# Performance work log

Hardware: AMD Instinct MI355X
Metric: run time of the kernel (lower is better)

The kernel has to match this reference:

```python
import jax, jax.numpy as jnp
import numpy as np

DIM = 256
NEG_SLOPE = 0.01  # torch F.leaky_relu default


def setup_inputs() -> dict:
    key = jax.random.key(0)
    ks = jax.random.split(key, 10)
    B, O, I, D = 16, 64, 512, DIM
    q = jax.random.normal(ks[0], (B, O, D), dtype=jnp.float32)
    k = jax.random.normal(ks[1], (B, I, D), dtype=jnp.float32)
    v = jax.random.normal(ks[2], (B, I, D), dtype=jnp.float32)
    mask = jax.random.randint(ks[3], (B, I), 0, 2).astype(bool)  # 1/True = pad
    s = 1.0 / np.sqrt(2 * D)
    # score MLP: Linear(2D -> D), tanh, Linear(D -> 1)
    W1 = jax.random.normal(ks[4], (D, 2 * D), dtype=jnp.float32) * s
    b1 = jnp.zeros((D,), dtype=jnp.float32)
    W2 = jax.random.normal(ks[5], (1, D), dtype=jnp.float32) * (1.0 / np.sqrt(D))
    b2 = jnp.zeros((1,), dtype=jnp.float32)
    # output projection fw: Linear(D -> D)
    Wf = jax.random.normal(ks[6], (D, D), dtype=jnp.float32) * (1.0 / np.sqrt(D))
    bf = jnp.zeros((D,), dtype=jnp.float32)
    return {"q": q, "k": k, "v": v, "mask": mask,
            "W1": W1, "b1": b1, "W2": W2, "b2": b2, "Wf": Wf, "bf": bf}


def reference(q, k, v, mask, W1, b1, W2, b2, Wf, bf):
    # Linear over concat([q, k]) decomposes exactly: W1 @ [q;k] = W1q@q + W1k@k
    D = q.shape[-1]
    W1q, W1k = W1[:, :D], W1[:, D:]
    qp = jnp.einsum('bod,hd->boh', q, W1q)          # (B, O, D)
    kp = jnp.einsum('bid,hd->bih', k, W1k)          # (B, I, D)
    h = jnp.tanh(qp[:, :, None, :] + kp[:, None, :, :] + b1)  # (B, O, I, D)
    score = jnp.einsum('boih,h->boi', h, W2[0]) + b2[0]       # (B, O, I)
    score = jnp.where(mask[:, None, :], -jnp.inf, score)
    attn = jax.nn.softmax(score, axis=-1)           # (B, O, I)
    out = jnp.einsum('boi,bid->bod', attn, v)       # (B, O, D)
    out = out @ Wf.T + bf                           # dropout in eval mode = identity
    out = jnp.where(out >= 0, out, NEG_SLOPE * out) # leaky_relu
    return out, attn
```

## Files before the change

kernel.cpp:

```cpp
#include <hip/hip_runtime.h>
#include <math.h>

#define DIM 256
#define BATCH 16
#define NO 64
#define NI 512
#define NIP 528
#define WFT_LD 272
#define NEG_SLOPE 0.01f
#define CSCALE 2.885390081777927f
#define OT 2

typedef float f32x4 __attribute__((ext_vector_type(4)));
typedef __bf16 bf16x8 __attribute__((ext_vector_type(8)));
typedef unsigned int u32x4 __attribute__((ext_vector_type(4)));

__device__ __forceinline__ void split2(float f, unsigned int& hi16, float& lo) {
  unsigned int u = __builtin_bit_cast(unsigned int, f);
  unsigned int h = (u + 0x7FFFu + ((u >> 16) & 1u)) & 0xFFFF0000u;
  hi16 = h >> 16;
  lo = f - __builtin_bit_cast(float, h);
}
__device__ __forceinline__ unsigned int rne16(float f) {
  unsigned int u = __builtin_bit_cast(unsigned int, f);
  return (u + 0x7FFFu + ((u >> 16) & 1u)) >> 16;
}

struct __align__(8) U2 { unsigned int x, y; };

#define OFF_AH 0
#define OFF_AL 9216
#define OFF_WH 18432
#define OFF_WL 27648

__global__ __launch_bounds__(256, 4) void proj_kernel(
    const float* __restrict__ q, const float* __restrict__ k,
    const float* __restrict__ W1, const float* __restrict__ b1,
    const float* __restrict__ Wf, const int* __restrict__ mask,
    float* __restrict__ Eq, float* __restrict__ Ek4, float* __restrict__ WfT)
{
  __shared__ __align__(16) char smemRaw[36864];
  __shared__ int idx_s[64];
  __shared__ int swtot[4];

  const int t  = threadIdx.x;
  const int bx = blockIdx.x;

  if (bx >= 576) {
    float* smem = (float*)smemRaw;
    const int tt = bx - 576;
    const int tr = tt >> 2, tc = tt & 3;
#pragma unroll
    for (int p = 0; p < 4; ++p) {
      int idx2 = p * 256 + t;
      int row = idx2 >> 4, j = idx2 & 15;
      float4 vv = *(const float4*)(Wf + (size_t)(tr * 64 + row) * 256 + tc * 64 + j * 4);
      *(float4*)&smem[row * 68 + j * 4] = vv;
    }
    __syncthreads();
#pragma unroll
    for (int p = 0; p < 4; ++p) {
      int idx2 = p * 256 + t;
      int row = idx2 >> 4, j = idx2 & 15;
      float4 ov;
      ov.x = smem[(j * 4 + 0) * 68 + row];
      ov.y = smem[(j * 4 + 1) * 68 + row];
      ov.z = smem[(j * 4 + 2) * 68 + row];
      ov.w = smem[(j * 4 + 3) * 68 + row];
      *(float4*)(WfT + (size_t)(tc * 64 + row) * WFT_LD + tr * 64 + j * 4) = ov;
    }
    return;
  }

  const int mt = bx >> 2;
  const int nt = bx & 3;
  const int h0 = nt * 64;
  const bool isq = (mt < 16);

  const int srow = t >> 4;
  const int sc4  = t & 15;
  const int lane = t & 63, w = t >> 6;
  const int m0w = (w >> 1) * 32, n0w = (w & 1) * 32;
  const int lr = lane & 15, lg = lane >> 4;

  const float* src;
  int coff, bb = 0, jb0 = 0, cntb = 0;
  int rowg[4];

  if (isq) {
    src  = q + (size_t)(mt * 64) * DIM;
    coff = 0;
#pragma unroll
    for (int p = 0; p < 4; ++p) rowg[p] = srow + p * 16;
  } else {
    const int ki = mt - 16;
    bb  = ki >> 3;
    jb0 = (ki & 7) * 64;
    const int e0 = (mask[bb * NI + 2 * t] == 0);
    const int e1 = (mask[bb * NI + 2 * t + 1] == 0);
    const int ps = e0 + e1;
    int x = ps;
#pragma unroll
    for (int off = 1; off < 64; off <<= 1) {
      int y = __shfl_up(x, off, 64);
      if (lane >= off) x += y;
    }
    if (lane == 63) swtot[w] = x;
    if (t < 64) idx_s[t] = 0;
    __syncthreads();
    int woffv = 0;
#pragma unroll
    for (int w2 = 0; w2 < 4; ++w2) {
      int v_ = swtot[w2];
      if (w2 < w) woffv += v_;
      cntb += v_;
    }
    const int excl = woffv + x - ps;
    const int p0 = excl, p1 = excl + e0;
    if (e0 && p0 >= jb0 && p0 < jb0 + 64) idx_s[p0 - jb0] = 2 * t;
    if (e1 && p1 >= jb0 && p1 < jb0 + 64) idx_s[p1 - jb0] = 2 * t + 1;
    __syncthreads();
    if (jb0 >= cntb) return;
    src  = k + (size_t)bb * NI * DIM;
    coff = DIM;
#pragma unroll
    for (int p = 0; p < 4; ++p) rowg[p] = idx_s[srow + p * 16];
  }

  f32x4 acc[2][2] = {};

  float4 aR[4], wR[4];
#define LOADC(c0_)                                                              \
  _Pragma("unroll")                                                             \
  for (int p = 0; p < 4; ++p) {                                                 \
    aR[p] = *(const float4*)(src + (size_t)rowg[p] * DIM + (c0_) + sc4 * 4);    \
    wR[p] = *(const float4*)(W1 + (size_t)(h0 + srow + p * 16) * (2 * DIM) + coff + (c0_) + sc4 * 4); \
  }

  LOADC(0)

  for (int c = 0; c < 4; ++c) {
#pragma unroll
    for (int p = 0; p < 4; ++p) {
      int row = srow + p * 16;
      int boff = row * 144 + sc4 * 8;
      unsigned int h0_, h1_, h2_, h3_;
      float l0, l1, l2, l3;
      split2(aR[p].x, h0_, l0); split2(aR[p].y, h1_, l1);
      split2(aR[p].z, h2_, l2); split2(aR[p].w, h3_, l3);
      *(U2*)(smemRaw + OFF_AH + boff) = { h0_ | (h1_ << 16), h2_ | (h3_ << 16) };
      *(U2*)(smemRaw + OFF_AL + boff) = { rne16(l0) | (rne16(l1) << 16),
                                          rne16(l2) | (rne16(l3) << 16) };
      split2(wR[p].x, h0_, l0); split2(wR[p].y, h1_, l1);
      split2(wR[p].z, h2_, l2); split2(wR[p].w, h3_, l3);
      *(U2*)(smemRaw + OFF_WH + boff) = { h0_ | (h1_ << 16), h2_ | (h3_ << 16) };
      *(U2*)(smemRaw + OFF_WL + boff) = { rne16(l0) | (rne16(l1) << 16),
                                          rne16(l2) | (rne16(l3) << 16) };
    }
    __syncthreads();

    if (c < 3) { LOADC((c + 1) * 64) }

#pragma unroll
    for (int kk = 0; kk < 2; ++kk) {
      const int kb = kk * 64 + lg * 16;
      bf16x8 ah[2], al[2], bh[2], bl[2];
#pragma unroll
      for (int mi = 0; mi < 2; ++mi) {
        int row = m0w + mi * 16 + lr;
        ah[mi] = __builtin_bit_cast(bf16x8, *(const u32x4*)(smemRaw + OFF_AH + row * 144 + kb));
        al[mi] = __builtin_bit_cast(bf16x8, *(const u32x4*)(smemRaw + OFF_AL + row * 144 + kb));
      }
#pragma unroll
      for (int ni = 0; ni < 2; ++ni) {
        int row = n0w + ni * 16 + lr;
        bh[ni] = __builtin_bit_cast(bf16x8, *(const u32x4*)(smemRaw + OFF_WH + row * 144 + kb));
        bl[ni] = __builtin_bit_cast(bf16x8, *(const u32x4*)(smemRaw + OFF_WL + row * 144 + kb));
      }
#pragma unroll
      for (int mi = 0; mi < 2; ++mi)
#pragma unroll
        for (int ni = 0; ni < 2; ++ni) {
          acc[mi][ni] = __builtin_amdgcn_mfma_f32_16x16x32_bf16(ah[mi], bh[ni], acc[mi][ni], 0, 0, 0);
          acc[mi][ni] = __builtin_amdgcn_mfma_f32_16x16x32_bf16(ah[mi], bl[ni], acc[mi][ni], 0, 0, 0);
          acc[mi][ni] = __builtin_amdgcn_mfma_f32_16x16x32_bf16(al[mi], bh[ni], acc[mi][ni], 0, 0, 0);
        }
    }
    __syncthreads();
  }

  if (isq) {
    const int r0 = mt * 64;
#pragma unroll
    for (int ni = 0; ni < 2; ++ni) {
      int h = h0 + n0w + ni * 16 + lr;
      float b1v = b1[h];
#pragma unroll
      for (int mi = 0; mi < 2; ++mi)
#pragma unroll
        for (int rg = 0; rg < 4; ++rg) {
          int r = r0 + m0w + mi * 16 + lg * 4 + rg;
          Eq[(size_t)r * DIM + h] =
              __builtin_amdgcn_exp2f((acc[mi][ni][rg] + b1v) * CSCALE);
        }
    }
  } else {
    const int lim = cntb - jb0;
#pragma unroll
    for (int mi = 0; mi < 2; ++mi)
#pragma unroll
      for (int rg = 0; rg < 4; ++rg) {
        int local = m0w + mi * 16 + lg * 4 + rg;
        if (local < lim) {
          int pos = jb0 + local;
#pragma unroll
          for (int ni = 0; ni < 2; ++ni) {
            int h = h0 + n0w + ni * 16 + lr;
            Ek4[((size_t)(bb * 64 + (h >> 2)) * NIP + pos) * 4 + (h & 3)] =
                __builtin_amdgcn_exp2f(acc[mi][ni][rg] * CSCALE);
          }
        }
      }
  }
}

__device__ __forceinline__ void f4arr(float4 v, float* a) {
  a[0] = v.x; a[1] = v.y; a[2] = v.z; a[3] = v.w;
}

__global__ __launch_bounds__(512, 4) void attn_kernel(
    const float* __restrict__ Eq, const float* __restrict__ Ek4,
    const float* __restrict__ v, const int* __restrict__ mask,
    const float* __restrict__ W2, const float* __restrict__ b2,
    const float* __restrict__ WfT, const float* __restrict__ bf,
    float* __restrict__ out, float* __restrict__ attn_out)
{
  __shared__ float sc[OT][NI];
  __shared__ int   idxs[NI];
  __shared__ float qs[OT][DIM];
  __shared__ float w2s[DIM];
  __shared__ float pvp[8][OT][DIM];
  __shared__ float o0[OT][DIM];
  __shared__ float red4[8][OT];
  __shared__ float redw[8];
  __shared__ int   swtot8[8];

  const int t    = threadIdx.x;
  const int lane = t & 63;
  const int wid  = t >> 6;

  const int blk  = blockIdx.x;
  const int tile = (blk & 7) * 64 + (blk >> 3);
  const int b    = tile >> 5;
  const int bo0  = b * 64 + (tile & 31) * OT;

  const int unm = (mask[b * NI + t] == 0) ? 1 : 0;
  unsigned long long bal = __ballot(unm);
  int my = __popcll(bal & ((1ull << lane) - 1ull));
  if (lane == 0) swtot8[wid] = __popcll(bal);

  if (t < 128) {
    const int r = t >> 6, part = t & 63;
    *(float4*)&qs[r][part * 4] =
        *(const float4*)(Eq + (size_t)(bo0 + r) * DIM + part * 4);
  } else if (t < 192) {
    const int part = t - 128;
    *(float4*)&w2s[part * 4] = *(const float4*)(W2 + part * 4);
  }

  float partial = (t < DIM) ? W2[t] : 0.f;
#pragma unroll
  for (int off = 32; off >= 1; off >>= 1) partial += __shfl_xor(partial, off, 64);
  if (lane == 0) redw[wid] = partial;
  __syncthreads();

  int cntb = 0, woffv = 0;
#pragma unroll
  for (int w = 0; w < 8; ++w) {
    int v_ = swtot8[w];
    if (w < wid) woffv += v_;
    cntb += v_;
  }
  const int myPos = unm ? (woffv + my) : -1;
  if (unm) idxs[myPos] = t;

  float sumw2 = 0.f;
#pragma unroll
  for (int w = 0; w < 8; ++w) sumw2 += redw[w];
  const float base = sumw2 + b2[0];

  const int j = t;
  const bool active = (j < cntb);
  const int jc = active ? j : (cntb > 0 ? cntb - 1 : 0);
  const float4* kb4 = (const float4*)Ek4 + (size_t)b * 64 * NIP;

  float acc0 = 0.f, acc1 = 0.f;
  if (wid * 64 < cntb) {
    const float4* kp = kb4 + jc;
#pragma unroll
    for (int c0 = 0; c0 < 64; c0 += 16) {
      float4 kqr[16];
#pragma unroll
      for (int u = 0; u < 16; ++u)
        kqr[u] = kp[(size_t)(c0 + u) * NIP];
#pragma unroll
      for (int u = 0; u < 16; ++u) {
        const int hq = c0 + u;
        float wr[4], q0r[4], q1r[4], kv[4];
        f4arr(*(const float4*)&w2s[hq * 4], wr);
        f4arr(*(const float4*)&qs[0][hq * 4], q0r);
        f4arr(*(const float4*)&qs[1][hq * 4], q1r);
        f4arr(kqr[u], kv);
#pragma unroll
        for (int pr = 0; pr < 2; ++pr) {
          const int ea = pr * 2, eb = pr * 2 + 1;
          float A0 = fmaf(q0r[ea], kv[ea], 1.f);
          float B0 = fmaf(q0r[eb], kv[eb], 1.f);
          float N0 = fmaf(wr[eb], A0, wr[ea] * B0);
          acc0 = fmaf(N0, __builtin_amdgcn_rcpf(A0 * B0), acc0);
          float A1 = fmaf(q1r[ea], kv[ea], 1.f);
          float B1 = fmaf(q1r[eb], kv[eb], 1.f);
          float N1 = fmaf(wr[eb], A1, wr[ea] * B1);
          acc1 = fmaf(N1, __builtin_amdgcn_rcpf(A1 * B1), acc1);
        }
      }
    }
  }

  float s0 = active ? (base - 2.f * acc0) : -INFINITY;
  float s1 = active ? (base - 2.f * acc1) : -INFINITY;

  float p0 = __builtin_amdgcn_exp2f(s0 * 1.4426950408889634f);
  float p1 = __builtin_amdgcn_exp2f(s1 * 1.4426950408889634f);
  float ps0 = p0, ps1 = p1;
#pragma unroll
  for (int off = 32; off >= 1; off >>= 1) {
    ps0 += __shfl_xor(ps0, off, 64);
    ps1 += __shfl_xor(ps1, off, 64);
  }
  __syncthreads();
  if (lane == 0) { red4[wid][0] = ps0; red4[wid][1] = ps1; }
  __syncthreads();
  float ss0 = 0.f, ss1 = 0.f;
#pragma unroll
  for (int w = 0; w < 8; ++w) { ss0 += red4[w][0]; ss1 += red4[w][1]; }
  const float a0 = p0 * __builtin_amdgcn_rcpf(ss0);
  const float a1 = p1 * __builtin_amdgcn_rcpf(ss1);
  sc[0][j] = a0;
  sc[1][j] = a1;
  __syncthreads();

  {
    float w0 = (myPos >= 0) ? sc[0][myPos] : 0.f;
    float w1 = (myPos >= 0) ? sc[1][myPos] : 0.f;
    attn_out[(size_t)(bo0 + 0) * NI + t] = w0;
    attn_out[(size_t)(bo0 + 1) * NI + t] = w1;
  }

  {
    const int d4 = lane;
    float4 av0 = {0.f, 0.f, 0.f, 0.f};
    float4 av1 = {0.f, 0.f, 0.f, 0.f};
    const float4* vb4 = (const float4*)(v + (size_t)b * NI * DIM);
    const int jstart = wid * 64;
    const int jend = min(jstart + 64, cntb);
    int jb = jstart;
    for (; jb + 8 <= jend; jb += 8) {
      float4 vr[8];
      float sa0[8], sa1[8];
#pragma unroll
      for (int u = 0; u < 8; ++u) {
        int row = idxs[jb + u];
        vr[u] = vb4[(size_t)row * 64 + d4];
        sa0[u] = sc[0][jb + u];
        sa1[u] = sc[1][jb + u];
      }
#pragma unroll
      for (int u = 0; u < 8; ++u) {
        av0.x = fmaf(sa0[u], vr[u].x, av0.x);
        av0.y = fmaf(sa0[u], vr[u].y, av0.y);
        av0.z = fmaf(sa0[u], vr[u].z, av0.z);
        av0.w = fmaf(sa0[u], vr[u].w, av0.w);
        av1.x = fmaf(sa1[u], vr[u].x, av1.x);
        av1.y = fmaf(sa1[u], vr[u].y, av1.y);
        av1.z = fmaf(sa1[u], vr[u].z, av1.z);
        av1.w = fmaf(sa1[u], vr[u].w, av1.w);
      }
    }
    for (; jb < jend; ++jb) {
      int row = idxs[jb];
      float sa0 = sc[0][jb], sa1 = sc[1][jb];
      float4 vv = vb4[(size_t)row * 64 + d4];
      av0.x = fmaf(sa0, vv.x, av0.x);
      av0.y = fmaf(sa0, vv.y, av0.y);
      av0.z = fmaf(sa0, vv.z, av0.z);
      av0.w = fmaf(sa0, vv.w, av0.w);
      av1.x = fmaf(sa1, vv.x, av1.x);
      av1.y = fmaf(sa1, vv.y, av1.y);
      av1.z = fmaf(sa1, vv.z, av1.z);
      av1.w = fmaf(sa1, vv.w, av1.w);
    }
    *(float4*)&pvp[wid][0][d4 * 4] = av0;
    *(float4*)&pvp[wid][1][d4 * 4] = av1;
  }
  __syncthreads();
  {
    int oo = t >> 8, d = t & 255;
    float sacc = 0.f;
#pragma unroll
    for (int w = 0; w < 8; ++w) sacc += pvp[w][oo][d];
    o0[oo][d] = sacc;
  }
  __syncthreads();

  if (t < DIM) {
    const int d = t;
    float f0 = 0.f, f1 = 0.f;
#pragma unroll
    for (int c0 = 0; c0 < 256; c0 += 16) {
      float wv[16];
#pragma unroll
      for (int u = 0; u < 16; ++u)
        wv[u] = WfT[(size_t)(c0 + u) * WFT_LD + d];
#pragma unroll
      for (int u = 0; u < 16; ++u) {
        f0 = fmaf(o0[0][c0 + u], wv[u], f0);
        f1 = fmaf(o0[1][c0 + u], wv[u], f1);
      }
    }
    float bfv = bf[d];
    f0 += bfv; f1 += bfv;
    f0 = (f0 >= 0.f) ? f0 : NEG_SLOPE * f0;
    f1 = (f1 >= 0.f) ? f1 : NEG_SLOPE * f1;
    out[(size_t)(bo0 + 0) * DIM + d] = f0;
    out[(size_t)(bo0 + 1) * DIM + d] = f1;
  }
}

extern "C" void kernel_launch(void* const* d_in, const int* in_sizes, int n_in,
                              void* d_out, int out_size, void* d_ws, size_t ws_size,
                              hipStream_t stream) {
  const float* q    = (const float*)d_in[0];
  const float* k    = (const float*)d_in[1];
  const float* v    = (const float*)d_in[2];
  const int*   mask = (const int*)d_in[3];
  const float* W1   = (const float*)d_in[4];
  const float* b1   = (const float*)d_in[5];
  const float* W2   = (const float*)d_in[6];
  const float* b2   = (const float*)d_in[7];
  const float* Wf   = (const float*)d_in[8];
  const float* bf   = (const float*)d_in[9];

  float* out      = (float*)d_out;
  float* attn_out = out + (size_t)BATCH * NO * DIM;

  float* Eq   = (float*)d_ws;
  float* Ek4  = Eq + (size_t)BATCH * NO * DIM;
  float* WfT  = Ek4 + (size_t)BATCH * 64 * NIP * 4;

  proj_kernel<<<592, 256, 0, stream>>>(q, k, W1, b1, Wf, mask, Eq, Ek4, WfT);
  attn_kernel<<<(BATCH * NO) / OT, 512, 0, stream>>>(Eq, Ek4, v, mask,
                                                     W2, b2, WfT, bf, out, attn_out);
}
```

Measured before the change: 121.8 us.

## Fuse projection and attention kernels into one persistent kernel with grid barrier

Merges the projection kernel and the attention kernel into a single 512-block launch. Each block first computes one or two projection tiles, reshaped for 512 threads, then waits on an atomic grid-wide barrier before running the attention phase. The goal is to remove the second kernel launch and the gap between the two kernels. The cost is a spin barrier that relies on all 512 blocks being co-resident, plus an extra memset launch and agent-scope stores.

```diff
diff --git a/kernel.cpp b/kernel.cpp
--- a/kernel.cpp
+++ b/kernel.cpp
@@ -10,6 +10,7 @@
 #define NEG_SLOPE 0.01f
 #define CSCALE 2.885390081777927f
 #define OT 2
+#define NBLK 512
 
 typedef float f32x4 __attribute__((ext_vector_type(4)));
 typedef __bf16 bf16x8 __attribute__((ext_vector_type(8)));
@@ -25,6 +26,12 @@
   unsigned int u = __builtin_bit_cast(unsigned int, f);
   return (u + 0x7FFFu + ((u >> 16) & 1u)) >> 16;
 }
+__device__ __forceinline__ void st_agent(float* p, float v) {
+  __hip_atomic_store(p, v, __ATOMIC_RELAXED, __HIP_MEMORY_SCOPE_AGENT);
+}
+__device__ __forceinline__ void f4arr(float4 v, float* a) {
+  a[0] = v.x; a[1] = v.y; a[2] = v.z; a[3] = v.w;
+}
 
 struct __align__(8) U2 { unsigned int x, y; };
 
@@ -32,130 +39,126 @@
 #define OFF_AL 9216
 #define OFF_WH 18432
 #define OFF_WL 27648
-
-__global__ __launch_bounds__(256, 4) void proj_kernel(
+#define OFF_IDX 36864
+#define OFF_SWT 37120
+
+__device__ void proj_tile(
+    int L, char* SMEM, int t, int lane, int wid,
     const float* __restrict__ q, const float* __restrict__ k,
     const float* __restrict__ W1, const float* __restrict__ b1,
     const float* __restrict__ Wf, const int* __restrict__ mask,
     float* __restrict__ Eq, float* __restrict__ Ek4, float* __restrict__ WfT)
 {
-  __shared__ __align__(16) char smemRaw[36864];
-  __shared__ int idx_s[64];
-  __shared__ int swtot[4];
-
-  const int t  = threadIdx.x;
-  const int bx = blockIdx.x;
-
-  if (bx >= 576) {
-    float* smem = (float*)smemRaw;
-    const int tt = bx - 576;
+  if (L >= 576) {
+    float* smem = (float*)SMEM;
+    const int tt = L - 576;
     const int tr = tt >> 2, tc = tt & 3;
 #pragma unroll
-    for (int p = 0; p < 4; ++p) {
-      int idx2 = p * 256 + t;
+    for (int p = 0; p < 2; ++p) {
+      int idx2 = p * 512 + t;
       int row = idx2 >> 4, j = idx2 & 15;
       float4 vv = *(const float4*)(Wf + (size_t)(tr * 64 + row) * 256 + tc * 64 + j * 4);
       *(float4*)&smem[row * 68 + j * 4] = vv;
     }
     __syncthreads();
 #pragma unroll
-    for (int p = 0; p < 4; ++p) {
-      int idx2 = p * 256 + t;
+    for (int p = 0; p < 2; ++p) {
+      int idx2 = p * 512 + t;
       int row = idx2 >> 4, j = idx2 & 15;
-      float4 ov;
-      ov.x = smem[(j * 4 + 0) * 68 + row];
-      ov.y = smem[(j * 4 + 1) * 68 + row];
-      ov.z = smem[(j * 4 + 2) * 68 + row];
-      ov.w = smem[(j * 4 + 3) * 68 + row];
-      *(float4*)(WfT + (size_t)(tc * 64 + row) * WFT_LD + tr * 64 + j * 4) = ov;
+      float* dst = WfT + (size_t)(tc * 64 + row) * WFT_LD + tr * 64 + j * 4;
+      st_agent(dst + 0, smem[(j * 4 + 0) * 68 + row]);
+      st_agent(dst + 1, smem[(j * 4 + 1) * 68 + row]);
+      st_agent(dst + 2, smem[(j * 4 + 2) * 68 + row]);
+      st_agent(dst + 3, smem[(j * 4 + 3) * 68 + row]);
     }
     return;
   }
 
-  const int mt = bx >> 2;
-  const int nt = bx & 3;
+  int mt, nt;
+  if (L < 64) { mt = L >> 2; nt = L & 3; }
+  else if (L < 512) {
+    int L2 = L - 64;
+    int kip = L2 >> 2;
+    int ki = (kip / 7) * 8 + (kip % 7);
+    mt = 16 + ki; nt = L2 & 3;
+  } else {
+    int L2 = L - 512;
+    int ki = ((L2 >> 2) << 3) + 7;
+    mt = 16 + ki; nt = L2 & 3;
+  }
+
   const int h0 = nt * 64;
   const bool isq = (mt < 16);
-
   const int srow = t >> 4;
   const int sc4  = t & 15;
-  const int lane = t & 63, w = t >> 6;
-  const int m0w = (w >> 1) * 32, n0w = (w & 1) * 32;
+  const int m0w = (wid >> 2) * 32, n0w = (wid & 3) * 16;
   const int lr = lane & 15, lg = lane >> 4;
+
+  int* idx_s = (int*)(SMEM + OFF_IDX);
+  int* swt   = (int*)(SMEM + OFF_SWT);
 
   const float* src;
   int coff, bb = 0, jb0 = 0, cntb = 0;
-  int rowg[4];
+  int rowg[2];
 
   if (isq) {
     src  = q + (size_t)(mt * 64) * DIM;
     coff = 0;
-#pragma unroll
-    for (int p = 0; p < 4; ++p) rowg[p] = srow + p * 16;
+    rowg[0] = srow; rowg[1] = srow + 32;
   } else {
     const int ki = mt - 16;
     bb  = ki >> 3;
     jb0 = (ki & 7) * 64;
-    const int e0 = (mask[bb * NI + 2 * t] == 0);
-    const int e1 = (mask[bb * NI + 2 * t + 1] == 0);
-    const int ps = e0 + e1;
-    int x = ps;
-#pragma unroll
-    for (int off = 1; off < 64; off <<= 1) {
-      int y = __shfl_up(x, off, 64);
-      if (lane >= off) x += y;
-    }
-    if (lane == 63) swtot[w] = x;
+    const int unm = (mask[bb * NI + t] == 0) ? 1 : 0;
+    unsigned long long bal = __ballot(unm);
+    int my = __popcll(bal & ((1ull << lane) - 1ull));
+    if (lane == 0) swt[wid] = __popcll(bal);
     if (t < 64) idx_s[t] = 0;
     __syncthreads();
     int woffv = 0;
 #pragma unroll
-    for (int w2 = 0; w2 < 4; ++w2) {
-      int v_ = swtot[w2];
-      if (w2 < w) woffv += v_;
+    for (int w2 = 0; w2 < 8; ++w2) {
+      int v_ = swt[w2];
+      if (w2 < wid) woffv += v_;
       cntb += v_;
     }
-    const int excl = woffv + x - ps;
-    const int p0 = excl, p1 = excl + e0;
-    if (e0 && p0 >= jb0 && p0 < jb0 + 64) idx_s[p0 - jb0] = 2 * t;
-    if (e1 && p1 >= jb0 && p1 < jb0 + 64) idx_s[p1 - jb0] = 2 * t + 1;
+    const int mp = unm ? (woffv + my) : -1;
+    if (mp >= jb0 && mp < jb0 + 64) idx_s[mp - jb0] = t;
     __syncthreads();
     if (jb0 >= cntb) return;
     src  = k + (size_t)bb * NI * DIM;
     coff = DIM;
-#pragma unroll
-    for (int p = 0; p < 4; ++p) rowg[p] = idx_s[srow + p * 16];
-  }
-
-  f32x4 acc[2][2] = {};
-
-  float4 aR[4], wR[4];
+    rowg[0] = idx_s[srow]; rowg[1] = idx_s[srow + 32];
+  }
+
+  f32x4 acc[2] = {};
+  float4 aR[2], wR[2];
 #define LOADC(c0_)                                                              \
   _Pragma("unroll")                                                             \
-  for (int p = 0; p < 4; ++p) {                                                 \
+  for (int p = 0; p < 2; ++p) {                                                 \
     aR[p] = *(const float4*)(src + (size_t)rowg[p] * DIM + (c0_) + sc4 * 4);    \
-    wR[p] = *(const float4*)(W1 + (size_t)(h0 + srow + p * 16) * (2 * DIM) + coff + (c0_) + sc4 * 4); \
+    wR[p] = *(const float4*)(W1 + (size_t)(h0 + srow + p * 32) * (2 * DIM) + coff + (c0_) + sc4 * 4); \
   }
 
   LOADC(0)
 
   for (int c = 0; c < 4; ++c) {
 #pragma unroll
-    for (int p = 0; p < 4; ++p) {
-      int row = srow + p * 16;
+    for (int p = 0; p < 2; ++p) {
+      int row = srow + p * 32;
       int boff = row * 144 + sc4 * 8;
       unsigned int h0_, h1_, h2_, h3_;
       float l0, l1, l2, l3;
       split2(aR[p].x, h0_, l0); split2(aR[p].y, h1_, l1);
       split2(aR[p].z, h2_, l2); split2(aR[p].w, h3_, l3);
-      *(U2*)(smemRaw + OFF_AH + boff) = { h0_ | (h1_ << 16), h2_ | (h3_ << 16) };
-      *(U2*)(smemRaw + OFF_AL + boff) = { rne16(l0) | (rne16(l1) << 16),
-                                          rne16(l2) | (rne16(l3) << 16) };
+      *(U2*)(SMEM + OFF_AH + boff) = { h0_ | (h1_ << 16), h2_ | (h3_ << 16) };
+      *(U2*)(SMEM + OFF_AL + boff) = { rne16(l0) | (rne16(l1) << 16),
+                                       rne16(l2) | (rne16(l3) << 16) };
       split2(wR[p].x, h0_, l0); split2(wR[p].y, h1_, l1);
       split2(wR[p].z, h2_, l2); split2(wR[p].w, h3_, l3);
-      *(U2*)(smemRaw + OFF_WH + boff) = { h0_ | (h1_ << 16), h2_ | (h3_ << 16) };
-      *(U2*)(smemRaw + OFF_WL + boff) = { rne16(l0) | (rne16(l1) << 16),
-                                          rne16(l2) | (rne16(l3) << 16) };
+      *(U2*)(SMEM + OFF_WH + boff) = { h0_ | (h1_ << 16), h2_ | (h3_ << 16) };
+      *(U2*)(SMEM + OFF_WL + boff) = { rne16(l0) | (rne16(l1) << 16),
+                                       rne16(l2) | (rne16(l3) << 16) };
     }
     __syncthreads();
 
@@ -164,46 +167,41 @@
 #pragma unroll
     for (int kk = 0; kk < 2; ++kk) {
       const int kb = kk * 64 + lg * 16;
-      bf16x8 ah[2], al[2], bh[2], bl[2];
+      bf16x8 ah[2], al[2], bh, bl;
 #pragma unroll
       for (int mi = 0; mi < 2; ++mi) {
         int row = m0w + mi * 16 + lr;
-        ah[mi] = __builtin_bit_cast(bf16x8, *(const u32x4*)(smemRaw + OFF_AH + row * 144 + kb));
-        al[mi] = __builtin_bit_cast(bf16x8, *(const u32x4*)(smemRaw + OFF_AL + row * 144 + kb));
-      }
-#pragma unroll
-      for (int ni = 0; ni < 2; ++ni) {
-        int row = n0w + ni * 16 + lr;
-        bh[ni] = __builtin_bit_cast(bf16x8, *(const u32x4*)(smemRaw + OFF_WH + row * 144 + kb));
-        bl[ni] = __builtin_bit_cast(bf16x8, *(const u32x4*)(smemRaw + OFF_WL + row * 144 + kb));
-      }
-#pragma unroll
-      for (int mi = 0; mi < 2; ++mi)
-#pragma unroll
-        for (int ni = 0; ni < 2; ++ni) {
-          acc[mi][ni] = __builtin_amdgcn_mfma_f32_16x16x32_bf16(ah[mi], bh[ni], acc[mi][ni], 0, 0, 0);
-          acc[mi][ni] = __builtin_amdgcn_mfma_f32_16x16x32_bf16(ah[mi], bl[ni], acc[mi][ni], 0, 0, 0);
-          acc[mi][ni] = __builtin_amdgcn_mfma_f32_16x16x32_bf16(al[mi], bh[ni], acc[mi][ni], 0, 0, 0);
-        }
-    }
-    __syncthreads();
-  }
-
+        ah[mi] = __builtin_bit_cast(bf16x8, *(const u32x4*)(SMEM + OFF_AH + row * 144 + kb));
+        al[mi] = __builtin_bit_cast(bf16x8, *(const u32x4*)(SMEM + OFF_AL + row * 144 + kb));
+      }
+      {
+        int row = n0w + lr;
+        bh = __builtin_bit_cast(bf16x8, *(const u32x4*)(SMEM + OFF_WH + row * 144 + kb));
+        bl = __builtin_bit_cast(bf16x8, *(const u32x4*)(SMEM + OFF_WL + row * 144 + kb));
+      }
+#pragma unroll
+      for (int mi = 0; mi < 2; ++mi) {
+        acc[mi] = __builtin_amdgcn_mfma_f32_16x16x32_bf16(ah[mi], bh, acc[mi], 0, 0, 0);
+        acc[mi] = __builtin_amdgcn_mfma_f32_16x16x32_bf16(ah[mi], bl, acc[mi], 0, 0, 0);
+        acc[mi] = __builtin_amdgcn_mfma_f32_16x16x32_bf16(al[mi], bh, acc[mi], 0, 0, 0);
+      }
+    }
+    __syncthreads();
+  }
+#undef LOADC
+
+  const int h = h0 + n0w + lr;
   if (isq) {
     const int r0 = mt * 64;
-#pragma unroll
-    for (int ni = 0; ni < 2; ++ni) {
-      int h = h0 + n0w + ni * 16 + lr;
-      float b1v = b1[h];
-#pragma unroll
-      for (int mi = 0; mi < 2; ++mi)
-#pragma unroll
-        for (int rg = 0; rg < 4; ++rg) {
-          int r = r0 + m0w + mi * 16 + lg * 4 + rg;
-          Eq[(size_t)r * DIM + h] =
-              __builtin_amdgcn_exp2f((acc[mi][ni][rg] + b1v) * CSCALE);
-        }
-    }
+    float b1v = b1[h];
+#pragma unroll
+    for (int mi = 0; mi < 2; ++mi)
+#pragma unroll
+      for (int rg = 0; rg < 4; ++rg) {
+        int r = r0 + m0w + mi * 16 + lg * 4 + rg;
+        st_agent(Eq + (size_t)r * DIM + h,
+                 __builtin_amdgcn_exp2f((acc[mi][rg] + b1v) * CSCALE));
+      }
   } else {
     const int lim = cntb - jb0;
 #pragma unroll
@@ -212,56 +210,72 @@
       for (int rg = 0; rg < 4; ++rg) {
         int local = m0w + mi * 16 + lg * 4 + rg;
         if (local < lim) {
-          int pos = jb0 + local;
-#pragma unroll
-          for (int ni = 0; ni < 2; ++ni) {
-            int h = h0 + n0w + ni * 16 + lr;
-            Ek4[((size_t)(bb * 64 + (h >> 2)) * NIP + pos) * 4 + (h & 3)] =
-                __builtin_amdgcn_exp2f(acc[mi][ni][rg] * CSCALE);
-          }
+          st_agent(Ek4 + ((size_t)(bb * 64 + (h >> 2)) * NIP + jb0 + local) * 4 + (h & 3),
+                   __builtin_amdgcn_exp2f(acc[mi][rg] * CSCALE));
         }
       }
   }
 }
 
-__device__ __forceinline__ void f4arr(float4 v, float* a) {
-  a[0] = v.x; a[1] = v.y; a[2] = v.z; a[3] = v.w;
-}
-
-__global__ __launch_bounds__(512, 4) void attn_kernel(
-    const float* __restrict__ Eq, const float* __restrict__ Ek4,
+__global__ __launch_bounds__(512, 4) void fused_kernel(
+    const float* __restrict__ q, const float* __restrict__ k,
     const float* __restrict__ v, const int* __restrict__ mask,
+    const float* __restrict__ W1, const float* __restrict__ b1,
     const float* __restrict__ W2, const float* __restrict__ b2,
-    const float* __restrict__ WfT, const float* __restrict__ bf,
-    float* __restrict__ out, float* __restrict__ attn_out)
+    const float* __restrict__ Wf, const float* __restrict__ bf,
+    float* __restrict__ out, float* __restrict__ attn_out,
+    float* __restrict__ Eq, float* __restrict__ Ek4, float* __restrict__ WfT,
+    int* __restrict__ bar)
 {
-  __shared__ float sc[OT][NI];
-  __shared__ int   idxs[NI];
-  __shared__ float qs[OT][DIM];
-  __shared__ float w2s[DIM];
-  __shared__ float pvp[8][OT][DIM];
-  __shared__ float o0[OT][DIM];
-  __shared__ float red4[8][OT];
-  __shared__ float redw[8];
-  __shared__ int   swtot8[8];
+  __shared__ __align__(16) char SMEM[37888];
 
   const int t    = threadIdx.x;
   const int lane = t & 63;
   const int wid  = t >> 6;
-
-  const int blk  = blockIdx.x;
-  const int tile = (blk & 7) * 64 + (blk >> 3);
+  const int bx   = blockIdx.x;
+
+  proj_tile(bx, SMEM, t, lane, wid, q, k, W1, b1, Wf, mask, Eq, Ek4, WfT);
+  if (bx < 80) {
+    __syncthreads();
+    proj_tile(512 + bx, SMEM, t, lane, wid, q, k, W1, b1, Wf, mask, Eq, Ek4, WfT);
+  }
+
+  __syncthreads();
+  __threadfence();
+  if (t == 0) {
+    __hip_atomic_fetch_add(bar, 1, __ATOMIC_ACQ_REL, __HIP_MEMORY_SCOPE_AGENT);
+    while (__hip_atomic_load(bar, __ATOMIC_ACQUIRE, __HIP_MEMORY_SCOPE_AGENT) < NBLK) {
+      __builtin_amdgcn_s_sleep(2);
+    }
+  }
+  __syncthreads();
+  __threadfence();
+
+  float* sc0  = (float*)(SMEM);
+  float* sc1  = (float*)(SMEM + 2048);
+  int*   idxs = (int*)(SMEM + 4096);
+  float* qs0  = (float*)(SMEM + 6144);
+  float* qs1  = (float*)(SMEM + 7168);
+  float* w2s  = (float*)(SMEM + 8192);
+  float* pvp  = (float*)(SMEM + 9216);
+  float* o0a  = (float*)(SMEM + 25600);
+  float* red4 = (float*)(SMEM + 27648);
+  float* redw = (float*)(SMEM + 27712);
+  int*   swt8 = (int*)(SMEM + 27744);
+
+  const int tile = (bx & 7) * 64 + (bx >> 3);
   const int b    = tile >> 5;
   const int bo0  = b * 64 + (tile & 31) * OT;
 
   const int unm = (mask[b * NI + t] == 0) ? 1 : 0;
   unsigned long long bal = __ballot(unm);
   int my = __popcll(bal & ((1ull << lane) - 1ull));
-  if (lane == 0) swtot8[wid] = __popcll(bal);
+  if (lane == 0) swt8[wid] = __popcll(bal);
 
   if (t < 128) {
     const int r = t >> 6, part = t & 63;
-    *(float4*)&qs[r][part * 4] =
+    float* dst = (r == 0) ? qs0 : qs1;
+    *(float4*)&dst[part * 4] =
         *(const float4*)(Eq + (size_t)(bo0 + r) * DIM + part * 4);
   } else if (t < 192) {
     const int part = t - 128;
@@ -277,7 +291,7 @@
   int cntb = 0, woffv = 0;
 #pragma unroll
   for (int w = 0; w < 8; ++w) {
-    int v_ = swtot8[w];
+    int v_ = swt8[w];
     if (w < wid) woffv += v_;
     cntb += v_;
   }
@@ -308,8 +322,8 @@
         const int hq = c0 + u;
         float wr[4], q0r[4], q1r[4], kv[4];
         f4arr(*(const float4*)&w2s[hq * 4], wr);
-        f4arr(*(const float4*)&qs[0][hq * 4], q0r);
-        f4arr(*(const float4*)&qs[1][hq * 4], q1r);
+        f4arr(*(const float4*)&qs0[hq * 4], q0r);
+        f4arr(*(const float4*)&qs1[hq * 4], q1r);
         f4arr(kqr[u], kv);
 #pragma unroll
         for (int pr = 0; pr < 2; ++pr) {
@@ -339,20 +353,20 @@
     ps1 += __shfl_xor(ps1, off, 64);
   }
   __syncthreads();
-  if (lane == 0) { red4[wid][0] = ps0; red4[wid][1] = ps1; }
+  if (lane == 0) { red4[wid * 2 + 0] = ps0; red4[wid * 2 + 1] = ps1; }
   __syncthreads();
   float ss0 = 0.f, ss1 = 0.f;
 #pragma unroll
-  for (int w = 0; w < 8; ++w) { ss0 += red4[w][0]; ss1 += red4[w][1]; }
+  for (int w = 0; w < 8; ++w) { ss0 += red4[w * 2 + 0]; ss1 += red4[w * 2 + 1]; }
   const float a0 = p0 * __builtin_amdgcn_rcpf(ss0);
   const float a1 = p1 * __builtin_amdgcn_rcpf(ss1);
-  sc[0][j] = a0;
-  sc[1][j] = a1;
+  sc0[j] = a0;
+  sc1[j] = a1;
   __syncthreads();
 
   {
-    float w0 = (myPos >= 0) ? sc[0][myPos] : 0.f;
-    float w1 = (myPos >= 0) ? sc[1][myPos] : 0.f;
+    float w0 = (myPos >= 0) ? sc0[myPos] : 0.f;
+    float w1 = (myPos >= 0) ? sc1[myPos] : 0.f;
     attn_out[(size_t)(bo0 + 0) * NI + t] = w0;
     attn_out[(size_t)(bo0 + 1) * NI + t] = w1;
   }
@@ -372,8 +386,8 @@
       for (int u = 0; u < 8; ++u) {
         int row = idxs[jb + u];
         vr[u] = vb4[(size_t)row * 64 + d4];
-        sa0[u] = sc[0][jb + u];
-        sa1[u] = sc[1][jb + u];
+        sa0[u] = sc0[jb + u];
+        sa1[u] = sc1[jb + u];
       }
 #pragma unroll
       for (int u = 0; u < 8; ++u) {
@@ -389,7 +403,7 @@
     }
     for (; jb < jend; ++jb) {
       int row = idxs[jb];
-      float sa0 = sc[0][jb], sa1 = sc[1][jb];
+      float sa0 = sc0[jb], sa1 = sc1[jb];
       float4 vv = vb4[(size_t)row * 64 + d4];
       av0.x = fmaf(sa0, vv.x, av0.x);
       av0.y = fmaf(sa0, vv.y, av0.y);
@@ -400,16 +414,16 @@
       av1.z = fmaf(sa1, vv.z, av1.z);
       av1.w = fmaf(sa1, vv.w, av1.w);
     }
-    *(float4*)&pvp[wid][0][d4 * 4] = av0;
-    *(float4*)&pvp[wid][1][d4 * 4] = av1;
+    *(float4*)&pvp[(wid * 2 + 0) * 256 + d4 * 4] = av0;
+    *(float4*)&pvp[(wid * 2 + 1) * 256 + d4 * 4] = av1;
   }
   __syncthreads();
   {
     int oo = t >> 8, d = t & 255;
     float sacc = 0.f;
 #pragma unroll
-    for (int w = 0; w < 8; ++w) sacc += pvp[w][oo][d];
-    o0[oo][d] = sacc;
+    for (int w = 0; w < 8; ++w) sacc += pvp[(w * 2 + oo) * 256 + d];
+    o0a[oo * 256 + d] = sacc;
   }
   __syncthreads();
 
@@ -424,8 +438,8 @@
         wv[u] = WfT[(size_t)(c0 + u) * WFT_LD + d];
 #pragma unroll
       for (int u = 0; u < 16; ++u) {
-        f0 = fmaf(o0[0][c0 + u], wv[u], f0);
-        f1 = fmaf(o0[1][c0 + u], wv[u], f1);
+        f0 = fmaf(o0a[c0 + u], wv[u], f0);
+        f1 = fmaf(o0a[256 + c0 + u], wv[u], f1);
       }
     }
     float bfv = bf[d];
@@ -457,8 +471,9 @@
   float* Eq   = (float*)d_ws;
   float* Ek4  = Eq + (size_t)BATCH * NO * DIM;
   float* WfT  = Ek4 + (size_t)BATCH * 64 * NIP * 4;
-
-  proj_kernel<<<592, 256, 0, stream>>>(q, k, W1, b1, Wf, mask, Eq, Ek4, WfT);
-  attn_kernel<<<(BATCH * NO) / OT, 512, 0, stream>>>(Eq, Ek4, v, mask,
-                                                     W2, b2, WfT, bf, out, attn_out);
-}
+  int*   bar  = (int*)(WfT + (size_t)DIM * WFT_LD);
+
+  hipMemsetAsync(bar, 0, 256, stream);
+  fused_kernel<<<NBLK, 512, 0, stream>>>(q, k, v, mask, W1, b1, W2, b2, Wf, bf,
+                                         out, attn_out, Eq, Ek4, WfT, bar);
+}
```

After: 344.9 us. 2.83x slower.
